# Kernel optimization log

Hardware: AMD Instinct MI355X
Metric: run time of the kernel (lower is better)

Reference implementation:

```python
import jax, jax.numpy as jnp
import numpy as np

MU = 2.0 ** -10  # sign-LMS weight adaptation step


def setup_inputs() -> dict:
    key = jax.random.key(0)
    # 16-bit-range hyperspectral cube [Z, Y, X]
    image = jax.random.normal(key, (202, 256, 256), dtype=jnp.float32) * 1000.0
    # adaptive predictor weights per band over P=3 previous bands, init 0
    w0 = jnp.zeros((202, 3), dtype=jnp.float32)
    return {"image": image, "w0": w0}


def reference(image, w0):
    Z, Y, X = image.shape
    P = w0.shape[1]
    max_val = 2.0 ** 15 - 1.0  # dynamic_range = 16
    min_val = -(2.0 ** 15)

    # Spectral neighborhood: previous P bands at the same (y, x), zero-padded.
    # (lossless mode => sample representatives == original samples, so
    #  cross-band dependence uses raw samples directly)
    nb = jnp.stack(
        [jnp.pad(image, ((p + 1, 0), (0, 0), (0, 0)))[:Z] for p in range(P)],
        axis=-1,
    )  # [Z, Y, X, P]

    s_flat = image.reshape(Z, Y * X)       # BSQ raster order within each band
    nb_flat = nb.reshape(Z, Y * X, P)

    def band_scan(w_init, s_z, nb_z):
        # Sequential adaptive prediction within one band (strict data dependency)
        def step(w, inp):
            s, n = inp
            pred = jnp.clip(jnp.dot(w, n), min_val, max_val)
            res = s - pred
            w_new = w + MU * jnp.sign(res) * n  # sign-LMS update
            return w_new, (pred, res)

        _, (preds, ress) = jax.lax.scan(step, w_init, (s_z, nb_z))
        return preds, ress

    preds, ress = jax.vmap(band_scan)(w0, s_flat, nb_flat)  # bands independent
    predictions = preds.reshape(Z, Y, X)
    residuals = ress.reshape(Z, Y, X)

    # Lossless: quantized residual == residual; map rounded residual to
    # non-negative index delta = 2q (q>=0) or -2q-1 (q<0)
    q = jnp.round(residuals).astype(jnp.int32)
    mapped_indices = jnp.where(q >= 0, 2 * q, -2 * q - 1)
    quantized_residuals = residuals
    sample_representatives = image
    reconstructed = predictions + quantized_residuals

    return (predictions, residuals, quantized_residuals, mapped_indices,
            sample_representatives, reconstructed)
```

## Files before the change

### kernel.cpp

```cpp
#include <hip/hip_runtime.h>
#include <stdint.h>

#define ZB 202
#define YX 65536
#define NTOT ((size_t)ZB * YX)
#define SS 128
#define NSS (YX / SS)

#define FPAD_DW 388
#define INB_DW  (64 * 129)
#define OUTB_DW (128 * 65)
#define IN0_B   (FPAD_DW * 4)
#define IN1_B   (IN0_B + INB_DW * 4)
#define OUT0_B  (IN1_B + INB_DW * 4)
#define OUT1_B  (OUT0_B + OUTB_DW * 4)

__device__ __forceinline__ constexpr float kMU() { return 0.0009765625f; }
#define MINV (-32768.0f)
#define MAXV (32767.0f)

typedef float v2f __attribute__((ext_vector_type(2)));

#define GL_LDS4(g, l)                                                     \
    __builtin_amdgcn_global_load_lds(                                     \
        (const __attribute__((address_space(1))) void*)(g),               \
        (__attribute__((address_space(3))) void*)(l), 4, 0, 0)

__global__ __launch_bounds__(512, 1) void scan_kernel(const float* __restrict__ img,
                                                      const float* __restrict__ w0g,
                                                      float* __restrict__ out) {
    __shared__ float lds_all[FPAD_DW + 2 * INB_DW + 2 * OUTB_DW];

    const int tid = threadIdx.x;
    const int lane = tid & 63;
    const int wv = tid >> 6;
    const int b = blockIdx.x;

    float* const o_pred = out;
    float* const o_res  = out + NTOT;
    float* const o_qres = out + 2 * NTOT;
    float* const o_map  = out + 3 * NTOT;
    float* const o_repr = out + 4 * NTOT;
    float* const o_rec  = out + 5 * NTOT;

    const uint32_t ldsb =
        (uint32_t)(size_t)(__attribute__((address_space(3))) float*)lds_all;

    const int band = 61 * b + lane - 3;
    const int wband = band < 0 ? 0 : (band > ZB - 1 ? ZB - 1 : band);
    float w0 = w0g[wband * 3 + 0];
    float w1 = w0g[wband * 3 + 1];
    float w2 = w0g[wband * 3 + 2];
    const uint32_t inA0 = ldsb + IN0_B + (uint32_t)((lane - 3) * 516);
    const uint32_t inA1 = inA0 + (uint32_t)(INB_DW * 4);
    const uint32_t outw0 = ldsb + OUT0_B + (uint32_t)(lane * 4);
    const uint32_t outw1 = outw0 + (uint32_t)(OUTB_DW * 4);
    v2f A1[16], A2[16], B1[16], B2[16];

    const int cmax = (b == 3) ? 21 : 63;
    float sA[9], sB[9], dA[9], dB[9];

    auto stage = [&](int st) {
        float* ib = lds_all + FPAD_DW + (st & 1) * INB_DW;
        const float* g0 = img + (size_t)st * SS;
        for (int c = wv - 1; c < 64; c += 7) {
            const int z = 61 * b + c - 3;
            if (z < 0 || z > ZB - 1) continue;
            const float* gp = g0 + (size_t)z * YX;
            float* lp = ib + c * 129;
            GL_LDS4(gp + lane, lp);
            GL_LDS4(gp + 64 + lane, lp + 64);
        }
    };
    auto pissue = [&](int Tp, int sel) {
        const uint32_t ob = ldsb + (uint32_t)(sel ? OUT1_B : OUT0_B)
                          + (uint32_t)(lane * 260);
#pragma unroll
        for (int k = 0; k < 9; ++k) {
            const int c = 2 + wv + 7 * k;
            const int cc = c <= cmax ? c : 3;
            const int zz = 61 * b + cc - 3;
            const float* sp = img + (size_t)zz * YX + Tp + lane;
            asm volatile("global_load_dword %0, %2, off\n\t"
                         "global_load_dword %1, %2, off offset:256"
                         : "=&v"(sA[k]), "=&v"(sB[k]) : "v"(sp));
            const uint32_t da = ob + (uint32_t)(cc * 4);
            asm volatile("ds_read_b32 %0, %2\n\t"
                         "ds_read_b32 %1, %2 offset:16640"
                         : "=&v"(dA[k]), "=&v"(dB[k]) : "v"(da));
        }
    };
    auto pstore = [&](int Tp) {
#pragma unroll
        for (int k = 0; k < 9; ++k) {
            const int c = 2 + wv + 7 * k;
            if (c > cmax) continue;
            const int zz = 61 * b + c - 3;
            const size_t o = (size_t)zz * YX + Tp + lane;
#pragma unroll
            for (int h = 0; h < 2; ++h) {
                const float dv = h ? dB[k] : dA[k];
                const float s = h ? sB[k] : sA[k];
                const size_t oo = o + (size_t)(h * 64);
                const float pred = fminf(fmaxf(dv, MINV), MAXV);
                const float res = __fsub_rn(s, pred);
                const int q = (int)rintf(res);
                const int m = (q >= 0) ? (2 * q) : (-2 * q - 1);
                o_pred[oo] = pred;
                o_res[oo] = res;
                o_qres[oo] = res;
                o_map[oo] = (float)m;
                o_repr[oo] = s;
                o_rec[oo] = __fadd_rn(pred, res);
            }
        }
    };

#define RTISSUE(PA, PB, aA_)                                                   \
    {                                                                          \
        const uint32_t aB_ = (aA_) + 1032;                                     \
        _Pragma("unroll") for (int i = 0; i < 16; ++i) {                       \
            asm volatile("ds_read2_b32 %0, %1 offset0:%c2 offset1:%c3"         \
                         : "=&v"(PA[i]) : "v"(aA_), "i"(i), "i"(i + 129));     \
            asm volatile("ds_read2_b32 %0, %1 offset0:%c2 offset1:%c3"         \
                         : "=&v"(PB[i]) : "v"(aB_), "i"(i), "i"(i + 129));     \
        }                                                                      \
    }
#define KWAIT()                                                                \
    {                                                                          \
        asm volatile("s_waitcnt lgkmcnt(0)" ::: "memory");                     \
        __builtin_amdgcn_sched_barrier(0);                                     \
    }
#define CP(PA, PB, st_)                                                        \
    {                                                                          \
        _Pragma("unroll") for (int i = 0; i < 16; ++i) {                       \
            const float nx = PA[i].x, ny = PA[i].y;                            \
            const float nz = PB[i].x, s_ = PB[i].y;                            \
            float d = __fadd_rn(                                               \
                __fadd_rn(__fmul_rn(w0, nz), __fmul_rn(w1, ny)),               \
                __fmul_rn(w2, nx));                                            \
            float sg = (s_ > d) ? kMU() : ((s_ < d) ? -kMU() : 0.0f);          \
            w0 = __builtin_fmaf(sg, nz, w0);                                   \
            w1 = __builtin_fmaf(sg, ny, w1);                                   \
            w2 = __builtin_fmaf(sg, nx, w2);                                   \
            asm volatile("ds_write_b32 %0, %1 offset:%c2"                      \
                         :: "v"(outw), "v"(d),                                 \
                            "i"(((st_) * 16 + i) * 260) : "memory");           \
        }                                                                      \
    }

    if (wv != 0) {
        if (b == 0 && wv == 1) {
            for (int buf = 0; buf < 2; ++buf)
                for (int c = 0; c < 3; ++c) {
                    float* r = lds_all + FPAD_DW + buf * INB_DW + c * 129;
                    r[lane] = 0.0f;
                    r[lane + 64] = 0.0f;
                }
        }
        stage(0);
        asm volatile("s_waitcnt vmcnt(0)" ::: "memory");
    }
    __syncthreads();

    for (int ss = 0; ss < NSS; ++ss) {
        if (wv == 0) {
            const uint32_t inA = (ss & 1) ? inA1 : inA0;
            const uint32_t outw = (ss & 1) ? outw1 : outw0;
            RTISSUE(A1, A2, inA); KWAIT();
            RTISSUE(B1, B2, inA + 64);  CP(A1, A2, 0); KWAIT();
            RTISSUE(A1, A2, inA + 128); CP(B1, B2, 1); KWAIT();
            RTISSUE(B1, B2, inA + 192); CP(A1, A2, 2); KWAIT();
            RTISSUE(A1, A2, inA + 256); CP(B1, B2, 3); KWAIT();
            RTISSUE(B1, B2, inA + 320); CP(A1, A2, 4); KWAIT();
            RTISSUE(A1, A2, inA + 384); CP(B1, B2, 5); KWAIT();
            RTISSUE(B1, B2, inA + 448); CP(A1, A2, 6); KWAIT();
            CP(B1, B2, 7);
        } else {
            if (ss > 0) pissue((ss - 1) * SS, (ss - 1) & 1);
            if (ss + 1 < NSS) stage(ss + 1);
            asm volatile("s_waitcnt vmcnt(0) lgkmcnt(0)" ::: "memory");
            __builtin_amdgcn_sched_barrier(0);
            if (ss > 0) pstore((ss - 1) * SS);
        }
        __syncthreads();
    }

    if (wv != 0) {
        pissue((NSS - 1) * SS, (NSS - 1) & 1);
        asm volatile("s_waitcnt vmcnt(0) lgkmcnt(0)" ::: "memory");
        __builtin_amdgcn_sched_barrier(0);
        pstore((NSS - 1) * SS);
    }

#undef RTISSUE
#undef KWAIT
#undef CP
}

extern "C" void kernel_launch(void* const* d_in, const int* in_sizes, int n_in,
                              void* d_out, int out_size, void* d_ws, size_t ws_size,
                              hipStream_t stream) {
    const float* img = (const float*)d_in[0];
    const float* w0g = (const float*)d_in[1];
    float* out = (float*)d_out;

    scan_kernel<<<4, 512, 0, stream>>>(img, w0g, out);
}
```

Measured before the change: 2.833 ms.

## Transpose LDS output buffer and pack predictor multiplies with v_pk_mul_f32

The staging buffer for predictions is transposed from [time][lane] to [lane][time] with a 129-dword padded row. The scan wave can then write two consecutive predictions per ds_write2_b32, halving LDS write instructions on the serial critical path. The two products of weights w1 and w2 are also issued as one packed v_pk_mul_f32, cutting VALU instructions in the dependent chain. The consumer waves' read addressing is adjusted to match, which may change bank conflict behaviour on the reader side.

```diff
diff --git a/kernel.cpp b/kernel.cpp
--- a/kernel.cpp
+++ b/kernel.cpp
@@ -9,7 +9,7 @@
 
 #define FPAD_DW 388
 #define INB_DW  (64 * 129)
-#define OUTB_DW (128 * 65)
+#define OUTB_DW (64 * 129)
 #define IN0_B   (FPAD_DW * 4)
 #define IN1_B   (IN0_B + INB_DW * 4)
 #define OUT0_B  (IN1_B + INB_DW * 4)
@@ -49,11 +49,12 @@
     const int band = 61 * b + lane - 3;
     const int wband = band < 0 ? 0 : (band > ZB - 1 ? ZB - 1 : band);
     float w0 = w0g[wband * 3 + 0];
-    float w1 = w0g[wband * 3 + 1];
-    float w2 = w0g[wband * 3 + 2];
+    v2f W21;
+    W21.x = w0g[wband * 3 + 2];
+    W21.y = w0g[wband * 3 + 1];
     const uint32_t inA0 = ldsb + IN0_B + (uint32_t)((lane - 3) * 516);
     const uint32_t inA1 = inA0 + (uint32_t)(INB_DW * 4);
-    const uint32_t outw0 = ldsb + OUT0_B + (uint32_t)(lane * 4);
+    const uint32_t outw0 = ldsb + OUT0_B + (uint32_t)(lane * 516);
     const uint32_t outw1 = outw0 + (uint32_t)(OUTB_DW * 4);
     v2f A1[16], A2[16], B1[16], B2[16];
 
@@ -74,7 +75,7 @@
     };
     auto pissue = [&](int Tp, int sel) {
         const uint32_t ob = ldsb + (uint32_t)(sel ? OUT1_B : OUT0_B)
-                          + (uint32_t)(lane * 260);
+                          + (uint32_t)(lane * 4);
 #pragma unroll
         for (int k = 0; k < 9; ++k) {
             const int c = 2 + wv + 7 * k;
@@ -84,9 +85,9 @@
             asm volatile("global_load_dword %0, %2, off\n\t"
                          "global_load_dword %1, %2, off offset:256"
                          : "=&v"(sA[k]), "=&v"(sB[k]) : "v"(sp));
-            const uint32_t da = ob + (uint32_t)(cc * 4);
+            const uint32_t da = ob + (uint32_t)(cc * 516);
             asm volatile("ds_read_b32 %0, %2\n\t"
-                         "ds_read_b32 %1, %2 offset:16640"
+                         "ds_read_b32 %1, %2 offset:256"
                          : "=&v"(dA[k]), "=&v"(dB[k]) : "v"(da));
         }
     };
@@ -131,21 +132,28 @@
         asm volatile("s_waitcnt lgkmcnt(0)" ::: "memory");                     \
         __builtin_amdgcn_sched_barrier(0);                                     \
     }
+#define STEP1(PA, PB, i_, dres_)                                               \
+    {                                                                          \
+        const float nz_ = PB[i_].x, s_ = PB[i_].y;                             \
+        v2f pr_;                                                               \
+        asm("v_pk_mul_f32 %0, %1, %2" : "=v"(pr_) : "v"(W21), "v"(PA[i_]));    \
+        dres_ = __fadd_rn(__fadd_rn(__fmul_rn(w0, nz_), pr_.y), pr_.x);        \
+        const float sg = (s_ > dres_) ? kMU()                                  \
+                         : ((s_ < dres_) ? -kMU() : 0.0f);                     \
+        w0 = __builtin_fmaf(sg, nz_, w0);                                      \
+        W21.y = __builtin_fmaf(sg, PA[i_].y, W21.y);                           \
+        W21.x = __builtin_fmaf(sg, PA[i_].x, W21.x);                           \
+    }
 #define CP(PA, PB, st_)                                                        \
     {                                                                          \
-        _Pragma("unroll") for (int i = 0; i < 16; ++i) {                       \
-            const float nx = PA[i].x, ny = PA[i].y;                            \
-            const float nz = PB[i].x, s_ = PB[i].y;                            \
-            float d = __fadd_rn(                                               \
-                __fadd_rn(__fmul_rn(w0, nz), __fmul_rn(w1, ny)),               \
-                __fmul_rn(w2, nx));                                            \
-            float sg = (s_ > d) ? kMU() : ((s_ < d) ? -kMU() : 0.0f);          \
-            w0 = __builtin_fmaf(sg, nz, w0);                                   \
-            w1 = __builtin_fmaf(sg, ny, w1);                                   \
-            w2 = __builtin_fmaf(sg, nx, w2);                                   \
-            asm volatile("ds_write_b32 %0, %1 offset:%c2"                      \
-                         :: "v"(outw), "v"(d),                                 \
-                            "i"(((st_) * 16 + i) * 260) : "memory");           \
+        _Pragma("unroll") for (int j = 0; j < 8; ++j) {                        \
+            float d0_, d1_;                                                    \
+            STEP1(PA, PB, (2 * j), d0_);                                       \
+            STEP1(PA, PB, (2 * j + 1), d1_);                                   \
+            asm volatile("ds_write2_b32 %0, %1, %2 offset0:%c3 offset1:%c4"    \
+                         :: "v"(outw), "v"(d0_), "v"(d1_),                     \
+                            "i"((st_) * 16 + 2 * j),                           \
+                            "i"((st_) * 16 + 2 * j + 1) : "memory");           \
         }                                                                      \
     }
 
@@ -195,6 +203,7 @@
 
 #undef RTISSUE
 #undef KWAIT
+#undef STEP1
 #undef CP
 }
 
```

New measurement: 2.650 ms. 6.5% less time.
